# Kernel optimization log

Measured on AMD Instinct MI355X. Metric: run time of the kernel, lower is better.

## Reference

```python
import jax, jax.numpy as jnp
import numpy as np
import math

B, N, D = 4, 16384, 256
M, H = 64, 8
HD = D // H

def setup_inputs() -> dict:
    key = jax.random.key(0)
    ks = jax.random.split(key, 5)
    s = 1.0 / math.sqrt(D)
    return {
        "x": jax.random.normal(ks[0], (B, N, D), dtype=jnp.float32),
        "Ws": jax.random.normal(ks[1], (M, D), dtype=jnp.float32) * s,
        "bs": jnp.zeros((M,), dtype=jnp.float32),
        "Wqkv": jax.random.normal(ks[2], (3 * D, D), dtype=jnp.float32) * s,
        "Wo": jax.random.normal(ks[3], (D, D), dtype=jnp.float32) * s,
        "bo": jnp.zeros((D,), dtype=jnp.float32),
    }

def reference(x, Ws, bs, Wqkv, Wo, bo):
    # slice weights: softmax over N (dim=1), matching the torch code exactly
    logits = jnp.einsum('bnd,md->bnm', x, Ws) + bs          # [B,N,M]
    weights = jax.nn.softmax(logits, axis=1)                # softmax over N
    # pooling: tokens[b,m,d] = sum_n w[b,n,m] * x[b,n,d]
    tokens = jnp.einsum('bnm,bnd->bmd', weights, x)         # [B,M,D]
    # qkv projection (no bias)
    qkv = jnp.einsum('bmd,ed->bme', tokens, Wqkv)           # [B,M,3D]
    qkv = qkv.reshape(B, M, 3, H, HD)
    q = qkv[:, :, 0].transpose(0, 2, 1, 3)                  # [B,H,M,HD]
    k = qkv[:, :, 1].transpose(0, 2, 1, 3)
    v = qkv[:, :, 2].transpose(0, 2, 1, 3)
    scale = 1.0 / math.sqrt(HD)
    attn = jax.nn.softmax(jnp.einsum('bhmd,bhkd->bhmk', q, k) * scale, axis=-1)
    token_out = jnp.einsum('bhmk,bhkd->bhmd', attn, v)      # [B,H,M,HD]
    token_out = token_out.transpose(0, 2, 1, 3).reshape(B, M, D)
    token_out = jnp.einsum('bmd,ed->bme', token_out, Wo) + bo
    # unpooling: out[b,n,d] = sum_m w[b,n,m] * token_out[b,m,d]
    out = jnp.einsum('bnm,bmd->bnd', weights, token_out)    # [B,N,D]
    return out
```

## Files before the change

### kernel.cpp

```cpp
#include <hip/hip_runtime.h>
#include <math.h>

constexpr int B = 4;
constexpr int N = 16384;
constexpr int D = 256;
constexpr int M = 64;
constexpr int H = 8;
constexpr int NSLOT = 128;

typedef __attribute__((ext_vector_type(8))) short short8;
typedef __attribute__((ext_vector_type(4))) float floatx4;

__device__ __forceinline__ float4 ld4(const float* p) {
  return *reinterpret_cast<const float4*>(p);
}
__device__ __forceinline__ unsigned short f2bf(float f) {
  unsigned u = __float_as_uint(f);
  unsigned r = (u + 0x7fffu + ((u >> 16) & 1u)) >> 16;
  return (unsigned short)r;
}
__device__ __forceinline__ uint2 pack8(float4 a, float4 b, unsigned* hi) {
  unsigned d0 = (unsigned)f2bf(a.x) | ((unsigned)f2bf(a.y) << 16);
  unsigned d1 = (unsigned)f2bf(a.z) | ((unsigned)f2bf(a.w) << 16);
  hi[0] = (unsigned)f2bf(b.x) | ((unsigned)f2bf(b.y) << 16);
  hi[1] = (unsigned)f2bf(b.z) | ((unsigned)f2bf(b.w) << 16);
  return make_uint2(d0, d1);
}

__global__ __launch_bounds__(256, 2) void k12_fused(
    const float* __restrict__ x, const float* __restrict__ Ws,
    const float* __restrict__ bs, unsigned short* __restrict__ En,
    float* __restrict__ denomP, float* __restrict__ tokensP) {
  __shared__ unsigned short Wt[64][264];
  __shared__ unsigned short EsT[64][70];
  __shared__ unsigned short XsT[256][70];
  __shared__ float red[64];
  const int b = blockIdx.y;
  const int nb0 = blockIdx.x * 128;
  const int tid = threadIdx.x;
  const int w = tid >> 6, l = tid & 63;
  const int l15 = l & 15;
  const int q8 = (l >> 4) * 8;
  const int r4 = (l >> 4) * 4;
  const int ar = w * 16 + l15;

  float4 fx0[16];
  {
    const float* xr = &x[((size_t)(b * N + nb0 + ar)) * D];
#pragma unroll
    for (int ks = 0; ks < 8; ++ks) {
      fx0[2 * ks] = ld4(&xr[ks * 32 + q8]);
      fx0[2 * ks + 1] = ld4(&xr[ks * 32 + q8 + 4]);
    }
  }
#pragma unroll
  for (int p = 0; p < 4; ++p) {
    const int i = p * 256 + tid;
    const int row = i >> 4;
    const int c16 = (i & 15) * 16;
    const float* wp = &Ws[(size_t)row * 256 + c16];
    float4 v0 = ld4(wp), v1 = ld4(wp + 4), v2 = ld4(wp + 8), v3 = ld4(wp + 12);
    unsigned hi[2];
    uint2 lo = pack8(v0, v1, hi);
    *reinterpret_cast<uint4*>(&Wt[row][c16]) = make_uint4(lo.x, lo.y, hi[0], hi[1]);
    lo = pack8(v2, v3, hi);
    *reinterpret_cast<uint4*>(&Wt[row][c16 + 8]) = make_uint4(lo.x, lo.y, hi[0], hi[1]);
  }
  if (tid < 64) red[tid] = 0.0f;
  __syncthreads();

  floatx4 acc2[16];
#pragma unroll
  for (int i = 0; i < 16; ++i) acc2[i] = {0.f, 0.f, 0.f, 0.f};

  float4 fx1[16];
  short8 afr0[8], afr1[8];
  floatx4 acc[4];

#define K12_CVT(FX, AFR)                                               \
  do {                                                                 \
    _Pragma("unroll") for (int ks = 0; ks < 8; ++ks) {                 \
      const float4 a0 = FX[2 * ks], a1 = FX[2 * ks + 1];               \
      short8 tt;                                                       \
      tt[0] = (short)f2bf(a0.x); tt[1] = (short)f2bf(a0.y);            \
      tt[2] = (short)f2bf(a0.z); tt[3] = (short)f2bf(a0.w);            \
      tt[4] = (short)f2bf(a1.x); tt[5] = (short)f2bf(a1.y);            \
      tt[6] = (short)f2bf(a1.z); tt[7] = (short)f2bf(a1.w);            \
      AFR[ks] = tt;                                                    \
    }                                                                  \
  } while (0)

#define K12_SCATTER(AFR)                                               \
  do {                                                                 \
    _Pragma("unroll") for (int ks = 0; ks < 8; ++ks)                   \
        _Pragma("unroll") for (int j = 0; j < 8; ++j)                  \
            XsT[ks * 32 + q8 + j][ar] = (unsigned short)AFR[ks][j];    \
  } while (0)

#define K12_LOGITS(AFR)                                                \
  do {                                                                 \
    _Pragma("unroll") for (int i = 0; i < 4; ++i)                      \
        acc[i] = {0.f, 0.f, 0.f, 0.f};                                 \
    _Pragma("unroll") for (int ks = 0; ks < 8; ++ks) {                 \
      _Pragma("unroll") for (int mt = 0; mt < 4; ++mt) {               \
        short8 bf =                                                    \
            *reinterpret_cast<short8*>(&Wt[mt * 16 + l15][ks * 32 + q8]); \
        acc[mt] = __builtin_amdgcn_mfma_f32_16x16x32_bf16(AFR[ks], bf, \
                                                          acc[mt], 0, 0, 0); \
      }                                                                \
    }                                                                  \
  } while (0)

#define K12_EPILOG(N0)                                                 \
  do {                                                                 \
    _Pragma("unroll") for (int mt = 0; mt < 4; ++mt) {                 \
      const int m = mt * 16 + l15;                                     \
      const float bsm = bs[m];                                         \
      float s = 0.0f;                                                  \
      _Pragma("unroll") for (int r = 0; r < 4; ++r) {                  \
        const int n = w * 16 + r4 + r;                                 \
        const float e = __expf(acc[mt][r] + bsm);                      \
        s += e;                                                        \
        const unsigned short eb = f2bf(e);                             \
        EsT[m][w * 16 + r4 + r] = eb;                                  \
        En[((size_t)(b * N + (N0) + n)) * M + m] = eb;                 \
      }                                                                \
      atomicAdd(&red[m], s);                                           \
    }                                                                  \
  } while (0)

#define K12_POOL()                                                     \
  do {                                                                 \
    _Pragma("unroll") for (int ks2 = 0; ks2 < 2; ++ks2) {              \
      const int nf = ks2 * 32 + q8;                                    \
      short8 a = *reinterpret_cast<short8*>(&EsT[w * 16 + l15][nf]);   \
      _Pragma("unroll") for (int dt4 = 0; dt4 < 16; ++dt4) {           \
        short8 bf = *reinterpret_cast<short8*>(&XsT[dt4 * 16 + l15][nf]); \
        acc2[dt4] = __builtin_amdgcn_mfma_f32_16x16x32_bf16(a, bf,     \
                                                            acc2[dt4], 0, 0, 0); \
      }                                                                \
    }                                                                  \
  } while (0)

  K12_CVT(fx0, afr0);
  {
    const float* xr = &x[((size_t)(b * N + nb0 + 64 + ar)) * D];
#pragma unroll
    for (int ks = 0; ks < 8; ++ks) {
      fx1[2 * ks] = ld4(&xr[ks * 32 + q8]);
      fx1[2 * ks + 1] = ld4(&xr[ks * 32 + q8 + 4]);
    }
  }
  K12_SCATTER(afr0);
  K12_LOGITS(afr0);
  K12_EPILOG(nb0);
  K12_CVT(fx1, afr1);
  __syncthreads();
  K12_POOL();
  __syncthreads();

  K12_SCATTER(afr1);
  K12_LOGITS(afr1);
  K12_EPILOG(nb0 + 64);
  __syncthreads();
  K12_POOL();

  if (tid < 64)
    denomP[((size_t)(b * NSLOT) + blockIdx.x) * M + tid] = red[tid];
  float* op = tokensP + ((size_t)(b * NSLOT + blockIdx.x) * M) * D;
#pragma unroll
  for (int dt4 = 0; dt4 < 16; ++dt4)
#pragma unroll
    for (int r = 0; r < 4; ++r)
      op[(w * 16 + r4 + r) * D + dt4 * 16 + l15] = acc2[dt4][r];
#undef K12_CVT
#undef K12_SCATTER
#undef K12_LOGITS
#undef K12_EPILOG
#undef K12_POOL
}

__global__ __launch_bounds__(256) void k2r_reduce(
    const float* __restrict__ tokensP, const float* __restrict__ denomP,
    unsigned short* __restrict__ tokensB, float* __restrict__ rdenom,
    float* __restrict__ tokO) {
  const int b = blockIdx.x >> 6;
  const int m = blockIdx.x & 63;
  const int d = threadIdx.x;
  tokO[(size_t)blockIdx.x * 256 + d] = 0.0f;
  const float* base = tokensP + ((size_t)(b * NSLOT) * M + m) * D + d;
  float s0 = 0.f, s1 = 0.f, s2 = 0.f, s3 = 0.f;
#pragma unroll 4
  for (int s = 0; s < NSLOT; s += 4) {
    s0 += base[(size_t)(s + 0) * M * D];
    s1 += base[(size_t)(s + 1) * M * D];
    s2 += base[(size_t)(s + 2) * M * D];
    s3 += base[(size_t)(s + 3) * M * D];
  }
  tokensB[((size_t)(b * M) + m) * D + d] = f2bf((s0 + s1) + (s2 + s3));
  if (d < 64) {
    float v = denomP[((size_t)(b * NSLOT) + d) * M + m] +
              denomP[((size_t)(b * NSLOT) + 64 + d) * M + m];
#pragma unroll
    for (int off = 32; off > 0; off >>= 1) v += __shfl_down(v, off);
    if (d == 0) rdenom[b * M + m] = 1.0f / v;
  }
}

__global__ __launch_bounds__(256) void k_fa(
    const unsigned short* __restrict__ tokensB, const float* __restrict__ Wqkv,
    const float* __restrict__ Wo, const float* __restrict__ rdenom,
    float* __restrict__ tokO) {
  __shared__ __align__(16) char smem[84480];
  unsigned short* const At = reinterpret_cast<unsigned short*>(smem);
  unsigned short* const Wq = reinterpret_cast<unsigned short*>(smem + 33792);
  float* const qt = reinterpret_cast<float*>(smem);
  float* const kt = reinterpret_cast<float*>(smem + 8704);
  float* const vv = reinterpret_cast<float*>(smem + 17408);
  float* const P  = reinterpret_cast<float*>(smem + 26624);
  float* const ao = reinterpret_cast<float*>(smem + 44032);
  const int b = blockIdx.x >> 3;
  const int h = blockIdx.x & 7;
  const int tid = threadIdx.x;
  const int w = tid >> 6, l = tid & 63;
  const int l15 = l & 15;
  const int q8 = (l >> 4) * 8;
  const int r4 = (l >> 4) * 4;

#pragma unroll
  for (int p = 0; p < 8; ++p) {
    const int u = p * 256 + tid;
    const int row = u >> 5;
    const int c = (u & 31) * 8;
    *reinterpret_cast<short8*>(&At[row * 264 + c]) =
        *reinterpret_cast<const short8*>(&tokensB[((size_t)(b * M + row)) * 256 + c]);
  }
#pragma unroll
  for (int p = 0; p < 6; ++p) {
    const int u = p * 256 + tid;
    const int row = u >> 4;
    const int c16 = (u & 15) * 16;
    const int eg = (row < 32) ? (h * 32 + row)
                 : (row < 64) ? (256 + h * 32 + row - 32)
                              : (512 + h * 32 + row - 64);
    const float* wp = &Wqkv[(size_t)eg * 256 + c16];
    float4 v0 = ld4(wp), v1 = ld4(wp + 4), v2 = ld4(wp + 8), v3 = ld4(wp + 12);
    unsigned hi[2];
    uint2 lo = pack8(v0, v1, hi);
    *reinterpret_cast<uint4*>(&Wq[row * 264 + c16]) =
        make_uint4(lo.x, lo.y, hi[0], hi[1]);
    lo = pack8(v2, v3, hi);
    *reinterpret_cast<uint4*>(&Wq[row * 264 + c16 + 8]) =
        make_uint4(lo.x, lo.y, hi[0], hi[1]);
  }
  float rcp4[4];
#pragma unroll
  for (int r = 0; r < 4; ++r)
    rcp4[r] = rdenom[b * M + w * 16 + r4 + r];
  __syncthreads();

  floatx4 acc[6] = {{0.f, 0.f, 0.f, 0.f}, {0.f, 0.f, 0.f, 0.f},
                    {0.f, 0.f, 0.f, 0.f}, {0.f, 0.f, 0.f, 0.f},
                    {0.f, 0.f, 0.f, 0.f}, {0.f, 0.f, 0.f, 0.f}};
  const int arow = w * 16 + l15;
#pragma unroll
  for (int ks = 0; ks < 8; ++ks) {
    short8 a = *reinterpret_cast<short8*>(&At[arow * 264 + ks * 32 + q8]);
#pragma unroll
    for (int et = 0; et < 6; ++et) {
      short8 bf = *reinterpret_cast<short8*>(&Wq[(et * 16 + l15) * 264 + ks * 32 + q8]);
      acc[et] = __builtin_amdgcn_mfma_f32_16x16x32_bf16(a, bf, acc[et], 0, 0, 0);
    }
  }
  short8 wof[4];
#pragma unroll
  for (int dt4 = 0; dt4 < 4; ++dt4) {
    const float* wp = &Wo[(size_t)(w * 64 + dt4 * 16 + l15) * 256 + h * 32 + q8];
    float4 v0 = ld4(wp), v1 = ld4(wp + 4);
    short8 tt;
    tt[0] = (short)f2bf(v0.x); tt[1] = (short)f2bf(v0.y);
    tt[2] = (short)f2bf(v0.z); tt[3] = (short)f2bf(v0.w);
    tt[4] = (short)f2bf(v1.x); tt[5] = (short)f2bf(v1.y);
    tt[6] = (short)f2bf(v1.z); tt[7] = (short)f2bf(v1.w);
    wof[dt4] = tt;
  }
  __syncthreads();

#pragma unroll
  for (int r = 0; r < 4; ++r) {
    const int m = w * 16 + r4 + r;
    const float rc = rcp4[r];
#pragma unroll
    for (int et = 0; et < 6; ++et) {
      const float val = acc[et][r] * rc;
      const int c = (et & 1) * 16 + l15;
      if (et < 2) qt[c * 68 + m] = val;
      else if (et < 4) kt[c * 68 + m] = val;
      else vv[m * 36 + c] = val;
    }
  }
  __syncthreads();

  {
    const int tm4 = (tid & 15) * 4;
    const int tn4 = (tid >> 4) * 4;
    float sacc[4][4] = {};
    for (int k = 0; k < 32; ++k) {
      float4 a4 = ld4(&qt[k * 68 + tn4]);
      float4 b4 = ld4(&kt[k * 68 + tm4]);
#pragma unroll
      for (int i = 0; i < 4; ++i) {
        const float av = (i == 0) ? a4.x : (i == 1) ? a4.y : (i == 2) ? a4.z : a4.w;
        sacc[i][0] = fmaf(av, b4.x, sacc[i][0]);
        sacc[i][1] = fmaf(av, b4.y, sacc[i][1]);
        sacc[i][2] = fmaf(av, b4.z, sacc[i][2]);
        sacc[i][3] = fmaf(av, b4.w, sacc[i][3]);
      }
    }
    const float scale = 0.17677669529663687f;
#pragma unroll
    for (int i = 0; i < 4; ++i)
      *reinterpret_cast<float4*>(&P[(tn4 + i) * 68 + tm4]) =
          make_float4(sacc[i][0] * scale, sacc[i][1] * scale,
                      sacc[i][2] * scale, sacc[i][3] * scale);
  }
  __syncthreads();
  if (tid < 64) {
    float mx = -1e30f;
    for (int j = 0; j < 64; ++j) mx = fmaxf(mx, P[tid * 68 + j]);
    float s = 0.0f;
    for (int j = 0; j < 64; ++j) {
      const float e = expf(P[tid * 68 + j] - mx);
      P[tid * 68 + j] = e;
      s += e;
    }
    const float r = 1.0f / s;
    for (int j = 0; j < 64; ++j) P[tid * 68 + j] *= r;
  }
  __syncthreads();
  if (tid < 128) {
    const int i0 = (tid >> 3) * 4;
    const int c0 = (tid & 7) * 4;
    float o[4][4] = {};
    for (int j = 0; j < 64; ++j) {
      float4 v4 = ld4(&vv[j * 36 + c0]);
#pragma unroll
      for (int ii = 0; ii < 4; ++ii) {
        const float p = P[(i0 + ii) * 68 + j];
        o[ii][0] = fmaf(p, v4.x, o[ii][0]);
        o[ii][1] = fmaf(p, v4.y, o[ii][1]);
        o[ii][2] = fmaf(p, v4.z, o[ii][2]);
        o[ii][3] = fmaf(p, v4.w, o[ii][3]);
      }
    }
#pragma unroll
    for (int ii = 0; ii < 4; ++ii)
#pragma unroll
      for (int jj = 0; jj < 4; ++jj) ao[(i0 + ii) * 36 + c0 + jj] = o[ii][jj];
  }
  __syncthreads();

  floatx4 acc2[4][4] = {{{0.f, 0.f, 0.f, 0.f}, {0.f, 0.f, 0.f, 0.f},
                         {0.f, 0.f, 0.f, 0.f}, {0.f, 0.f, 0.f, 0.f}},
                        {{0.f, 0.f, 0.f, 0.f}, {0.f, 0.f, 0.f, 0.f},
                         {0.f, 0.f, 0.f, 0.f}, {0.f, 0.f, 0.f, 0.f}},
                        {{0.f, 0.f, 0.f, 0.f}, {0.f, 0.f, 0.f, 0.f},
                         {0.f, 0.f, 0.f, 0.f}, {0.f, 0.f, 0.f, 0.f}},
                        {{0.f, 0.f, 0.f, 0.f}, {0.f, 0.f, 0.f, 0.f},
                         {0.f, 0.f, 0.f, 0.f}, {0.f, 0.f, 0.f, 0.f}}};
#pragma unroll
  for (int mt = 0; mt < 4; ++mt) {
    short8 af;
#pragma unroll
    for (int j = 0; j < 8; ++j)
      af[j] = (short)f2bf(ao[(mt * 16 + l15) * 36 + q8 + j]);
#pragma unroll
    for (int dt4 = 0; dt4 < 4; ++dt4)
      acc2[mt][dt4] =
          __builtin_amdgcn_mfma_f32_16x16x32_bf16(af, wof[dt4], acc2[mt][dt4], 0, 0, 0);
  }
#pragma unroll
  for (int mt = 0; mt < 4; ++mt)
#pragma unroll
    for (int dt4 = 0; dt4 < 4; ++dt4)
#pragma unroll
      for (int r = 0; r < 4; ++r) {
        const int m = mt * 16 + r4 + r;
        const int d = w * 64 + dt4 * 16 + l15;
        atomicAdd(&tokO[((size_t)(b * M + m)) * D + d], acc2[mt][dt4][r]);
      }
}

__global__ __launch_bounds__(512, 4) void k6_unpool(
    const unsigned short* __restrict__ En, const float* __restrict__ tokO,
    const float* __restrict__ rdenom, const float* __restrict__ bo,
    float* __restrict__ out) {
  __shared__ unsigned short EnS[256][72];
  __shared__ unsigned short TpS[64][72];
  const int dt = blockIdx.x, nt = blockIdx.y, b = blockIdx.z;
  const int n0 = nt * 256, d0 = dt * 64;
  const int tid = threadIdx.x;
  const int w = tid >> 6, l = tid & 63;
  const int l15 = l & 15;
  const int q8 = (l >> 4) * 8;
#pragma unroll
  for (int p = 0; p < 4; ++p) {
    const int g = p * 512 + tid;
    const int row = g >> 3;
    const int c8 = (g & 7) * 8;
    *reinterpret_cast<short8*>(&EnS[row][c8]) =
        *reinterpret_cast<const short8*>(
            &En[((size_t)(b * N + n0 + row)) * M + c8]);
  }
  {
    const int m = tid >> 3;
    const int c8 = (tid & 7) * 8;
    const float rc = rdenom[b * M + m];
    const float* tp = &tokO[((size_t)(b * M + m)) * D + d0 + c8];
    float4 v0 = ld4(tp);
    float4 v1 = ld4(tp + 4);
    float4 bb0 = ld4(&bo[d0 + c8]);
    float4 bb1 = ld4(&bo[d0 + c8 + 4]);
    TpS[c8 + 0][m] = f2bf((v0.x + bb0.x) * rc);
    TpS[c8 + 1][m] = f2bf((v0.y + bb0.y) * rc);
    TpS[c8 + 2][m] = f2bf((v0.z + bb0.z) * rc);
    TpS[c8 + 3][m] = f2bf((v0.w + bb0.w) * rc);
    TpS[c8 + 4][m] = f2bf((v1.x + bb1.x) * rc);
    TpS[c8 + 5][m] = f2bf((v1.y + bb1.y) * rc);
    TpS[c8 + 6][m] = f2bf((v1.z + bb1.z) * rc);
    TpS[c8 + 7][m] = f2bf((v1.w + bb1.w) * rc);
  }
  __syncthreads();
#pragma unroll
  for (int pass = 0; pass < 2; ++pass) {
    const int arow = pass * 128 + w * 16 + l15;
    floatx4 acc[4] = {{0.f, 0.f, 0.f, 0.f},
                      {0.f, 0.f, 0.f, 0.f},
                      {0.f, 0.f, 0.f, 0.f},
                      {0.f, 0.f, 0.f, 0.f}};
#pragma unroll
    for (int ks = 0; ks < 2; ++ks) {
      short8 a = *reinterpret_cast<short8*>(&EnS[arow][ks * 32 + q8]);
#pragma unroll
      for (int dtile = 0; dtile < 4; ++dtile) {
        short8 bf = *reinterpret_cast<short8*>(
            &TpS[dtile * 16 + l15][ks * 32 + q8]);
        acc[dtile] =
            __builtin_amdgcn_mfma_f32_16x16x32_bf16(a, bf, acc[dtile], 0, 0, 0);
      }
    }
#pragma unroll
    for (int dtile = 0; dtile < 4; ++dtile)
#pragma unroll
      for (int r = 0; r < 4; ++r) {
        const int n = n0 + pass * 128 + w * 16 + (l >> 4) * 4 + r;
        const int d = d0 + dtile * 16 + l15;
        out[((size_t)(b * N + n)) * D + d] = acc[dtile][r];
      }
  }
}

extern "C" void kernel_launch(void* const* d_in, const int* in_sizes, int n_in,
                              void* d_out, int out_size, void* d_ws,
                              size_t ws_size, hipStream_t stream) {
  const float* x = (const float*)d_in[0];
  const float* Ws = (const float*)d_in[1];
  const float* bs = (const float*)d_in[2];
  const float* Wqkv = (const float*)d_in[3];
  const float* Wo = (const float*)d_in[4];
  const float* bo = (const float*)d_in[5];
  float* out = (float*)d_out;

  char* p = (char*)d_ws;
  unsigned short* En = (unsigned short*)p;  p += (size_t)B * N * M * 2;
  float* tokensP = (float*)p;               p += (size_t)B * NSLOT * M * D * 4;
  float* denomP = (float*)p;                p += (size_t)B * NSLOT * M * 4;
  float* rdenom = (float*)p;                p += (size_t)B * M * 4;
  unsigned short* tokensB = (unsigned short*)p; p += (size_t)B * M * D * 2;
  float* tokO = (float*)p;                  p += (size_t)B * M * D * 4;

  k12_fused<<<dim3(N / 128, B), 256, 0, stream>>>(x, Ws, bs, En, denomP,
                                                  tokensP);
  k2r_reduce<<<dim3(B * M), 256, 0, stream>>>(tokensP, denomP, tokensB,
                                              rdenom, tokO);
  k_fa<<<dim3(B * H), 256, 0, stream>>>(tokensB, Wqkv, Wo, rdenom, tokO);
  k6_unpool<<<dim3(D / 64, N / 256, B), 512, 0, stream>>>(En, tokO, rdenom, bo,
                                                          out);
}
```

Baseline: 166.9 us.

## Warp-specialize fused pooling kernel into producer and consumer waves with double buffering

Result: faster. 163.3 us (-2.1%).

```diff
diff --git a/kernel.cpp b/kernel.cpp
--- a/kernel.cpp
+++ b/kernel.cpp
@@ -6,7 +6,7 @@
 constexpr int D = 256;
 constexpr int M = 64;
 constexpr int H = 8;
-constexpr int NSLOT = 128;
+constexpr int NSLOT = 64;
 
 typedef __attribute__((ext_vector_type(8))) short short8;
 typedef __attribute__((ext_vector_type(4))) float floatx4;
@@ -27,35 +27,40 @@
   return make_uint2(d0, d1);
 }
 
-__global__ __launch_bounds__(256, 2) void k12_fused(
+__global__ __launch_bounds__(512, 2) void k12_fused(
     const float* __restrict__ x, const float* __restrict__ Ws,
     const float* __restrict__ bs, unsigned short* __restrict__ En,
     float* __restrict__ denomP, float* __restrict__ tokensP) {
   __shared__ unsigned short Wt[64][264];
-  __shared__ unsigned short EsT[64][70];
-  __shared__ unsigned short XsT[256][70];
+  __shared__ unsigned short EsT[2][64][70];
+  __shared__ unsigned short XsT[2][256][70];
   __shared__ float red[64];
   const int b = blockIdx.y;
-  const int nb0 = blockIdx.x * 128;
+  const int nb0 = blockIdx.x * 256;
   const int tid = threadIdx.x;
   const int w = tid >> 6, l = tid & 63;
   const int l15 = l & 15;
   const int q8 = (l >> 4) * 8;
   const int r4 = (l >> 4) * 4;
-  const int ar = w * 16 + l15;
-
-  float4 fx0[16];
-  {
+  const bool prod = (w < 4);
+  const int pw = w & 3;
+  const int ar = pw * 16 + l15;
+
+  float4 fxA[16], fxB[16];
+  short8 afr[8];
+  floatx4 acc[4];
+
+  if (prod) {
     const float* xr = &x[((size_t)(b * N + nb0 + ar)) * D];
 #pragma unroll
     for (int ks = 0; ks < 8; ++ks) {
-      fx0[2 * ks] = ld4(&xr[ks * 32 + q8]);
-      fx0[2 * ks + 1] = ld4(&xr[ks * 32 + q8 + 4]);
-    }
-  }
-#pragma unroll
-  for (int p = 0; p < 4; ++p) {
-    const int i = p * 256 + tid;
+      fxA[2 * ks] = ld4(&xr[ks * 32 + q8]);
+      fxA[2 * ks + 1] = ld4(&xr[ks * 32 + q8 + 4]);
+    }
+  }
+#pragma unroll
+  for (int p = 0; p < 2; ++p) {
+    const int i = p * 512 + tid;
     const int row = i >> 4;
     const int c16 = (i & 15) * 16;
     const float* wp = &Ws[(size_t)row * 256 + c16];
@@ -73,11 +78,7 @@
 #pragma unroll
   for (int i = 0; i < 16; ++i) acc2[i] = {0.f, 0.f, 0.f, 0.f};
 
-  float4 fx1[16];
-  short8 afr0[8], afr1[8];
-  floatx4 acc[4];
-
-#define K12_CVT(FX, AFR)                                               \
+#define K12_CVT(FX)                                                    \
   do {                                                                 \
     _Pragma("unroll") for (int ks = 0; ks < 8; ++ks) {                 \
       const float4 a0 = FX[2 * ks], a1 = FX[2 * ks + 1];               \
@@ -86,18 +87,27 @@
       tt[2] = (short)f2bf(a0.z); tt[3] = (short)f2bf(a0.w);            \
       tt[4] = (short)f2bf(a1.x); tt[5] = (short)f2bf(a1.y);            \
       tt[6] = (short)f2bf(a1.z); tt[7] = (short)f2bf(a1.w);            \
-      AFR[ks] = tt;                                                    \
+      afr[ks] = tt;                                                    \
     }                                                                  \
   } while (0)
 
-#define K12_SCATTER(AFR)                                               \
+#define K12_PREF(FX, NOFF)                                             \
+  do {                                                                 \
+    const float* xr = &x[((size_t)(b * N + (NOFF) + ar)) * D];         \
+    _Pragma("unroll") for (int ks = 0; ks < 8; ++ks) {                 \
+      FX[2 * ks] = ld4(&xr[ks * 32 + q8]);                             \
+      FX[2 * ks + 1] = ld4(&xr[ks * 32 + q8 + 4]);                     \
+    }                                                                  \
+  } while (0)
+
+#define K12_SCATTER(BUF)                                               \
   do {                                                                 \
     _Pragma("unroll") for (int ks = 0; ks < 8; ++ks)                   \
         _Pragma("unroll") for (int j = 0; j < 8; ++j)                  \
-            XsT[ks * 32 + q8 + j][ar] = (unsigned short)AFR[ks][j];    \
+            XsT[BUF][ks * 32 + q8 + j][ar] = (unsigned short)afr[ks][j]; \
   } while (0)
 
-#define K12_LOGITS(AFR)                                                \
+#define K12_LOGITS()                                                   \
   do {                                                                 \
     _Pragma("unroll") for (int i = 0; i < 4; ++i)                      \
         acc[i] = {0.f, 0.f, 0.f, 0.f};                                 \
@@ -105,75 +115,94 @@
       _Pragma("unroll") for (int mt = 0; mt < 4; ++mt) {               \
         short8 bf =                                                    \
             *reinterpret_cast<short8*>(&Wt[mt * 16 + l15][ks * 32 + q8]); \
-        acc[mt] = __builtin_amdgcn_mfma_f32_16x16x32_bf16(AFR[ks], bf, \
+        acc[mt] = __builtin_amdgcn_mfma_f32_16x16x32_bf16(afr[ks], bf, \
                                                           acc[mt], 0, 0, 0); \
       }                                                                \
     }                                                                  \
   } while (0)
 
-#define K12_EPILOG(N0)                                                 \
+#define K12_EPILOG(N0, BUF)                                            \
   do {                                                                 \
     _Pragma("unroll") for (int mt = 0; mt < 4; ++mt) {                 \
       const int m = mt * 16 + l15;                                     \
       const float bsm = bs[m];                                         \
       float s = 0.0f;                                                  \
       _Pragma("unroll") for (int r = 0; r < 4; ++r) {                  \
-        const int n = w * 16 + r4 + r;                                 \
+        const int n = pw * 16 + r4 + r;                                \
         const float e = __expf(acc[mt][r] + bsm);                      \
         s += e;                                                        \
         const unsigned short eb = f2bf(e);                             \
-        EsT[m][w * 16 + r4 + r] = eb;                                  \
+        EsT[BUF][m][pw * 16 + r4 + r] = eb;                            \
         En[((size_t)(b * N + (N0) + n)) * M + m] = eb;                 \
       }                                                                \
       atomicAdd(&red[m], s);                                           \
     }                                                                  \
   } while (0)
 
-#define K12_POOL()                                                     \
+#define K12_POOL(BUF)                                                  \
   do {                                                                 \
     _Pragma("unroll") for (int ks2 = 0; ks2 < 2; ++ks2) {              \
       const int nf = ks2 * 32 + q8;                                    \
-      short8 a = *reinterpret_cast<short8*>(&EsT[w * 16 + l15][nf]);   \
+      short8 a = *reinterpret_cast<short8*>(&EsT[BUF][pw * 16 + l15][nf]); \
       _Pragma("unroll") for (int dt4 = 0; dt4 < 16; ++dt4) {           \
-        short8 bf = *reinterpret_cast<short8*>(&XsT[dt4 * 16 + l15][nf]); \
+        short8 bf = *reinterpret_cast<short8*>(&XsT[BUF][dt4 * 16 + l15][nf]); \
         acc2[dt4] = __builtin_amdgcn_mfma_f32_16x16x32_bf16(a, bf,     \
                                                             acc2[dt4], 0, 0, 0); \
       }                                                                \
     }                                                                  \
   } while (0)
 
-  K12_CVT(fx0, afr0);
-  {
-    const float* xr = &x[((size_t)(b * N + nb0 + 64 + ar)) * D];
-#pragma unroll
-    for (int ks = 0; ks < 8; ++ks) {
-      fx1[2 * ks] = ld4(&xr[ks * 32 + q8]);
-      fx1[2 * ks + 1] = ld4(&xr[ks * 32 + q8 + 4]);
-    }
-  }
-  K12_SCATTER(afr0);
-  K12_LOGITS(afr0);
-  K12_EPILOG(nb0);
-  K12_CVT(fx1, afr1);
-  __syncthreads();
-  K12_POOL();
-  __syncthreads();
-
-  K12_SCATTER(afr1);
-  K12_LOGITS(afr1);
-  K12_EPILOG(nb0 + 64);
-  __syncthreads();
-  K12_POOL();
+  if (prod) {
+    K12_CVT(fxA);
+    K12_PREF(fxB, nb0 + 64);
+    K12_SCATTER(0);
+    K12_LOGITS();
+    K12_EPILOG(nb0, 0);
+  }
+  __syncthreads();
+  if (prod) {
+    K12_CVT(fxB);
+    K12_PREF(fxA, nb0 + 128);
+    K12_SCATTER(1);
+    K12_LOGITS();
+    K12_EPILOG(nb0 + 64, 1);
+  } else {
+    K12_POOL(0);
+  }
+  __syncthreads();
+  if (prod) {
+    K12_CVT(fxA);
+    K12_PREF(fxB, nb0 + 192);
+    K12_SCATTER(0);
+    K12_LOGITS();
+    K12_EPILOG(nb0 + 128, 0);
+  } else {
+    K12_POOL(1);
+  }
+  __syncthreads();
+  if (prod) {
+    K12_CVT(fxB);
+    K12_SCATTER(1);
+    K12_LOGITS();
+    K12_EPILOG(nb0 + 192, 1);
+  } else {
+    K12_POOL(0);
+  }
+  __syncthreads();
+  if (!prod) K12_POOL(1);
 
   if (tid < 64)
     denomP[((size_t)(b * NSLOT) + blockIdx.x) * M + tid] = red[tid];
-  float* op = tokensP + ((size_t)(b * NSLOT + blockIdx.x) * M) * D;
-#pragma unroll
-  for (int dt4 = 0; dt4 < 16; ++dt4)
-#pragma unroll
-    for (int r = 0; r < 4; ++r)
-      op[(w * 16 + r4 + r) * D + dt4 * 16 + l15] = acc2[dt4][r];
+  if (!prod) {
+    float* op = tokensP + ((size_t)(b * NSLOT + blockIdx.x) * M) * D;
+#pragma unroll
+    for (int dt4 = 0; dt4 < 16; ++dt4)
+#pragma unroll
+      for (int r = 0; r < 4; ++r)
+        op[(pw * 16 + r4 + r) * D + dt4 * 16 + l15] = acc2[dt4][r];
+  }
 #undef K12_CVT
+#undef K12_PREF
 #undef K12_SCATTER
 #undef K12_LOGITS
 #undef K12_EPILOG
@@ -199,8 +228,7 @@
   }
   tokensB[((size_t)(b * M) + m) * D + d] = f2bf((s0 + s1) + (s2 + s3));
   if (d < 64) {
-    float v = denomP[((size_t)(b * NSLOT) + d) * M + m] +
-              denomP[((size_t)(b * NSLOT) + 64 + d) * M + m];
+    float v = denomP[((size_t)(b * NSLOT) + d) * M + m];
 #pragma unroll
     for (int off = 32; off > 0; off >>= 1) v += __shfl_down(v, off);
     if (d == 0) rdenom[b * M + m] = 1.0f / v;
@@ -479,7 +507,7 @@
   unsigned short* tokensB = (unsigned short*)p; p += (size_t)B * M * D * 2;
   float* tokO = (float*)p;                  p += (size_t)B * M * D * 4;
 
-  k12_fused<<<dim3(N / 128, B), 256, 0, stream>>>(x, Ws, bs, En, denomP,
+  k12_fused<<<dim3(N / 256, B), 512, 0, stream>>>(x, Ws, bs, En, denomP,
                                                   tokensP);
   k2r_reduce<<<dim3(B * M), 256, 0, stream>>>(tokensP, denomP, tokensB,
                                               rdenom, tokO);
```
